# Kernel optimization log

Hardware: AMD Instinct MI355X
Metric: run time of the kernel (lower is better)

Reference implementation:

```python
import jax, jax.numpy as jnp
import numpy as np

N = 50000          # nodes
E = 800000         # edges per view (avg degree 16)
HID = 128
EMB = 64
K = 10
INPUT_DIMS = [1000, 800, 600]


def setup_inputs() -> dict:
    key = jax.random.key(0)
    ks = jax.random.split(key, 32)
    d = {}
    for i, din in enumerate(INPUT_DIMS):
        d[f"x{i}"] = jax.random.normal(ks[i], (N, din), jnp.float32)
        d[f"rows{i}"] = jax.random.randint(ks[3 + i], (E,), 0, N)
        d[f"cols{i}"] = jax.random.randint(ks[6 + i], (E,), 0, N)
        d[f"vals{i}"] = jax.random.uniform(ks[9 + i], (E,), jnp.float32)
        s1 = 1.0 / np.sqrt(HID)   # GraphConvolution.reset_parameters: 1/sqrt(out_features)
        s2 = 1.0 / np.sqrt(EMB)
        d[f"w1_{i}"] = jax.random.uniform(ks[12 + i], (din, HID), jnp.float32, -s1, s1)
        d[f"b1_{i}"] = jax.random.uniform(ks[15 + i], (HID,), jnp.float32, -s1, s1)
        d[f"w2_{i}"] = jax.random.uniform(ks[18 + i], (HID, EMB), jnp.float32, -s2, s2)
        d[f"b2_{i}"] = jax.random.uniform(ks[21 + i], (EMB,), jnp.float32, -s2, s2)
    sf = 1.0 / np.sqrt(EMB * 3)   # nn.Linear default init
    d["fusion_w"] = jax.random.uniform(ks[24], (EMB * 3, EMB), jnp.float32, -sf, sf)
    d["fusion_b"] = jax.random.uniform(ks[25], (EMB,), jnp.float32, -sf, sf)
    xav = np.sqrt(2.0 / (K + EMB))  # xavier_normal_
    d["cluster"] = jax.random.normal(ks[26], (K, EMB), jnp.float32) * xav
    return d


def _spmm(rows, cols, vals, dense):
    # adj (COO, NxN) @ dense [N, F] -> [N, F]
    return jax.ops.segment_sum(vals[:, None] * dense[cols], rows, num_segments=N)


def _encode(x, rows, cols, vals, w1, b1, w2, b2):
    h = jax.nn.relu(_spmm(rows, cols, vals, x @ w1) + b1)
    # F.dropout in eval mode = identity
    return _spmm(rows, cols, vals, h @ w2) + b2


def reference(x0, x1, x2,
              rows0, cols0, vals0,
              rows1, cols1, vals1,
              rows2, cols2, vals2,
              w1_0, b1_0, w2_0, b2_0,
              w1_1, b1_1, w2_1, b2_1,
              w1_2, b1_2, w2_2, b2_2,
              fusion_w, fusion_b, cluster):
    z0 = _encode(x0, rows0, cols0, vals0, w1_0, b1_0, w2_0, b2_0)
    z1 = _encode(x1, rows1, cols1, vals1, w1_1, b1_1, w2_1, b2_1)
    z2 = _encode(x2, rows2, cols2, vals2, w1_2, b1_2, w2_2, b2_2)
    z_concat = jnp.concatenate([z0, z1, z2], axis=1)          # [N, 3*EMB]
    z_fused = jax.nn.relu(z_concat @ fusion_w + fusion_b)     # [N, EMB]
    # DEC-style soft assignment (Student-t, alpha=1 -> exponent (1+1)/2 = 1)
    d2 = jnp.sum((z_fused[:, None, :] - cluster[None, :, :]) ** 2, axis=2)  # [N, K]
    q = 1.0 / (1.0 + d2)
    q = q / jnp.sum(q, axis=1, keepdims=True)
    return (z0, z1, z2, z_fused, q)
```

## Files before the change

kernel.cpp:

```cpp
#include <hip/hip_runtime.h>


#define N_NODES 50000
#define N_EDGES 800000
#define HID 128
#define EMB 64
#define NCLU 10

using bf16x8 = __attribute__((ext_vector_type(8))) short;
using f32x4  = __attribute__((ext_vector_type(4))) float;

static __device__ __forceinline__ unsigned short f2bf(float f) {
    unsigned int u = __float_as_uint(f);
    unsigned int r = (u + 0x7FFF + ((u >> 16) & 1)) >> 16;
    return (unsigned short)r;
}
static __device__ __forceinline__ float bflo(unsigned int t) {
    return __uint_as_float(t << 16);
}
static __device__ __forceinline__ float bfhi(unsigned int t) {
    return __uint_as_float(t & 0xFFFF0000u);
}


__global__ void hist3_kernel(const int* __restrict__ r0, const int* __restrict__ r1,
                             const int* __restrict__ r2, int* __restrict__ counts) {
    int t = blockIdx.x * 256 + threadIdx.x;
    int view = t / N_EDGES;
    int i = t - view * N_EDGES;
    const int* rp = (view == 0) ? r0 : (view == 1) ? r1 : r2;
    atomicAdd(&counts[view * N_NODES + rp[i]], 1);
}

__global__ __launch_bounds__(256) void scan1_kernel(
    const int* __restrict__ counts, int* __restrict__ tmp, int* __restrict__ bsum, int n)
{
    __shared__ int wt[4];
    int t = threadIdx.x, b = blockIdx.x;
    int i = b * 256 + t;
    int lane = t & 63, wid = t >> 6;
    int v = (i < n) ? counts[i] : 0;
    int incl = v;
    #pragma unroll
    for (int d = 1; d < 64; d <<= 1) {
        int u = __shfl_up(incl, d, 64);
        if (lane >= d) incl += u;
    }
    if (lane == 63) wt[wid] = incl;
    __syncthreads();
    int woff = 0;
    #pragma unroll
    for (int w = 0; w < 4; ++w) if (w < wid) woff += wt[w];
    if (i < n) tmp[i] = woff + incl - v;
    if (t == 255) bsum[b] = woff + incl;
}

__global__ __launch_bounds__(256) void scan2_kernel(
    const int* __restrict__ bsum, int* __restrict__ boff, int nb,
    int* __restrict__ row_ptr, int n)
{
    __shared__ int wt[4];
    int t = threadIdx.x;
    int lane = t & 63, wid = t >> 6;
    int carry = 0;
    for (int c0 = 0; c0 < nb; c0 += 256) {
        int i = c0 + t;
        int v = (i < nb) ? bsum[i] : 0;
        int incl = v;
        #pragma unroll
        for (int d = 1; d < 64; d <<= 1) {
            int u = __shfl_up(incl, d, 64);
            if (lane >= d) incl += u;
        }
        __syncthreads();
        if (lane == 63) wt[wid] = incl;
        __syncthreads();
        int woff = 0;
        #pragma unroll
        for (int w = 0; w < 4; ++w) if (w < wid) woff += wt[w];
        int chunktot = wt[0] + wt[1] + wt[2] + wt[3];
        if (i < nb) boff[i] = carry + woff + incl - v;
        carry += chunktot;
    }
    if (t == 0) row_ptr[n] = carry;
}

__global__ __launch_bounds__(256) void scan3_kernel(
    const int* __restrict__ tmp, const int* __restrict__ boff,
    int* __restrict__ row_ptr, int* __restrict__ cursor, int n)
{
    int i = blockIdx.x * 256 + threadIdx.x;
    if (i < n) {
        int e = tmp[i] + boff[blockIdx.x];
        row_ptr[i] = e;
        cursor[i] = e;
    }
}

__global__ void scatter3_kernel(
    const int* __restrict__ r0, const int* __restrict__ c0, const float* __restrict__ v0,
    const int* __restrict__ r1, const int* __restrict__ c1, const float* __restrict__ v1,
    const int* __restrict__ r2, const int* __restrict__ c2, const float* __restrict__ v2,
    int* __restrict__ cursor, float2* __restrict__ cv)
{
    int t = blockIdx.x * 256 + threadIdx.x;
    int view = t / N_EDGES;
    int i = t - view * N_EDGES;
    const int* rp = (view == 0) ? r0 : (view == 1) ? r1 : r2;
    const int* cp = (view == 0) ? c0 : (view == 1) ? c1 : c2;
    const float* vp = (view == 0) ? v0 : (view == 1) ? v1 : v2;
    int r = view * N_NODES + rp[i];
    int p = atomicAdd(&cursor[r], 1);
    float2 e;
    e.x = __uint_as_float((unsigned int)cp[i]);
    e.y = vp[i];
    cv[p] = e;
}


__global__ void wconv_kernel(const float* __restrict__ w, unsigned short* __restrict__ wt,
                             int din, int dinp) {
    int t = blockIdx.x * 256 + threadIdx.x;
    if (t >= 128 * dinp) return;
    int n = t / dinp, k = t - n * dinp;
    float f = (k < din) ? w[(size_t)k * 128 + n] : 0.f;
    wt[(size_t)n * dinp + k] = f2bf(f);
}


#define SAW 72

__global__ __launch_bounds__(256) void gemm1_kernel(
    const float* __restrict__ x, const unsigned short* __restrict__ w1t,
    unsigned short* __restrict__ xw, int Nn, int din, int dinp)
{
    __shared__ unsigned short As[64 * SAW];
    __shared__ unsigned short Bs[128 * SAW];
    int tid = threadIdx.x;
    int lane = tid & 63, wid = tid >> 6;
    int row0 = blockIdx.x * 64;
    int numK = dinp >> 6;

    int ar = tid >> 4;
    int ak = (tid & 15) * 4;
    float4 apre[4];
    uint4  bpre[4];

    auto loadA = [&](int k0) {
        #pragma unroll
        for (int p = 0; p < 4; ++p) {
            int r = p * 16 + ar;
            int gr = row0 + r;
            int k = k0 + ak;
            float4 v = make_float4(0.f, 0.f, 0.f, 0.f);
            if (gr < Nn) {
                if (k + 4 <= din) {
                    v = *(const float4*)(x + (size_t)gr * din + k);
                } else {
                    float e0 = (k + 0 < din) ? x[(size_t)gr * din + k + 0] : 0.f;
                    float e1 = (k + 1 < din) ? x[(size_t)gr * din + k + 1] : 0.f;
                    float e2 = (k + 2 < din) ? x[(size_t)gr * din + k + 2] : 0.f;
                    float e3 = (k + 3 < din) ? x[(size_t)gr * din + k + 3] : 0.f;
                    v = make_float4(e0, e1, e2, e3);
                }
            }
            apre[p] = v;
        }
    };
    auto loadB = [&](int k0) {
        #pragma unroll
        for (int p = 0; p < 4; ++p) {
            int idx = p * 256 + tid;
            int n = idx >> 3, q = idx & 7;
            bpre[p] = *(const uint4*)(w1t + (size_t)n * dinp + k0 + q * 8);
        }
    };
    auto storeLDS = [&]() {
        #pragma unroll
        for (int p = 0; p < 4; ++p) {
            int r = p * 16 + ar;
            ushort4 b;
            b.x = f2bf(apre[p].x); b.y = f2bf(apre[p].y);
            b.z = f2bf(apre[p].z); b.w = f2bf(apre[p].w);
            *(ushort4*)(&As[r * SAW + ak]) = b;
        }
        #pragma unroll
        for (int p = 0; p < 4; ++p) {
            int idx = p * 256 + tid;
            int n = idx >> 3, q = idx & 7;
            *(uint4*)(&Bs[n * SAW + q * 8]) = bpre[p];
        }
    };

    loadA(0); loadB(0);
    storeLDS();

    int kq = (lane >> 4) * 8;
    int sub = lane & 15;
    f32x4 acc[4][2] = {};
    for (int kt = 0;;) {
        __syncthreads();
        bool more = (kt + 1 < numK);
        if (more) { loadA((kt + 1) << 6); loadB((kt + 1) << 6); }
        #pragma unroll
        for (int kh = 0; kh < 2; ++kh) {
            bf16x8 af[4], bfr[2];
            #pragma unroll
            for (int mt = 0; mt < 4; ++mt)
                af[mt] = *(const bf16x8*)(&As[(mt * 16 + sub) * SAW + kh * 32 + kq]);
            #pragma unroll
            for (int nt = 0; nt < 2; ++nt)
                bfr[nt] = *(const bf16x8*)(&Bs[(wid * 32 + nt * 16 + sub) * SAW + kh * 32 + kq]);
            #pragma unroll
            for (int mt = 0; mt < 4; ++mt)
                #pragma unroll
                for (int nt = 0; nt < 2; ++nt)
                    acc[mt][nt] = __builtin_amdgcn_mfma_f32_16x16x32_bf16(af[mt], bfr[nt], acc[mt][nt], 0, 0, 0);
        }
        if (!more) break;
        __syncthreads();
        storeLDS();
        ++kt;
    }

    #pragma unroll
    for (int mt = 0; mt < 4; ++mt) {
        #pragma unroll
        for (int nt = 0; nt < 2; ++nt) {
            int col = wid * 32 + nt * 16 + (lane & 15);
            #pragma unroll
            for (int r = 0; r < 4; ++r) {
                int row = row0 + mt * 16 + (lane >> 4) * 4 + r;
                if (row < Nn) xw[(size_t)row * 128 + col] = f2bf(acc[mt][nt][r]);
            }
        }
    }
}


__global__ __launch_bounds__(256) void spmm128_kernel(
    const unsigned short* __restrict__ src, const int* __restrict__ row_ptr,
    const float2* __restrict__ cv, const float* __restrict__ bias,
    unsigned short* __restrict__ dst)
{
    const unsigned int* srcu = (const unsigned int*)src;
    int lane = threadIdx.x & 63;
    int r = blockIdx.x * 4 + (threadIdx.x >> 6);
    int s = row_ptr[r], e = row_ptr[r + 1];
    float a0 = 0.f, a1 = 0.f, b0 = 0.f, b1 = 0.f;
    int j = s;
    for (; j + 8 <= e; j += 8) {
        float2 p0 = cv[j], p1 = cv[j + 1], p2 = cv[j + 2], p3 = cv[j + 3];
        float2 p4 = cv[j + 4], p5 = cv[j + 5], p6 = cv[j + 6], p7 = cv[j + 7];
        unsigned int t0 = srcu[(size_t)__float_as_uint(p0.x) * 64 + lane];
        unsigned int t1 = srcu[(size_t)__float_as_uint(p1.x) * 64 + lane];
        unsigned int t2 = srcu[(size_t)__float_as_uint(p2.x) * 64 + lane];
        unsigned int t3 = srcu[(size_t)__float_as_uint(p3.x) * 64 + lane];
        unsigned int t4 = srcu[(size_t)__float_as_uint(p4.x) * 64 + lane];
        unsigned int t5 = srcu[(size_t)__float_as_uint(p5.x) * 64 + lane];
        unsigned int t6 = srcu[(size_t)__float_as_uint(p6.x) * 64 + lane];
        unsigned int t7 = srcu[(size_t)__float_as_uint(p7.x) * 64 + lane];
        a0 += p0.y * bflo(t0); a1 += p0.y * bfhi(t0);
        b0 += p1.y * bflo(t1); b1 += p1.y * bfhi(t1);
        a0 += p2.y * bflo(t2); a1 += p2.y * bfhi(t2);
        b0 += p3.y * bflo(t3); b1 += p3.y * bfhi(t3);
        a0 += p4.y * bflo(t4); a1 += p4.y * bfhi(t4);
        b0 += p5.y * bflo(t5); b1 += p5.y * bfhi(t5);
        a0 += p6.y * bflo(t6); a1 += p6.y * bfhi(t6);
        b0 += p7.y * bflo(t7); b1 += p7.y * bfhi(t7);
    }
    for (; j < e; ++j) {
        float2 p = cv[j];
        unsigned int t = srcu[(size_t)__float_as_uint(p.x) * 64 + lane];
        a0 += p.y * bflo(t); a1 += p.y * bfhi(t);
    }
    a0 += b0 + bias[lane * 2];
    a1 += b1 + bias[lane * 2 + 1];
    a0 = fmaxf(a0, 0.f); a1 = fmaxf(a1, 0.f);
    unsigned int o = (unsigned int)f2bf(a0) | ((unsigned int)f2bf(a1) << 16);
    ((unsigned int*)dst)[(size_t)r * 64 + lane] = o;
}


__global__ __launch_bounds__(256) void spmm64_kernel(
    const unsigned short* __restrict__ src, const int* __restrict__ row_ptr,
    const float2* __restrict__ cv, const float* __restrict__ bias,
    float* __restrict__ dst)
{
    int lane = threadIdx.x & 63;
    int r = blockIdx.x * 4 + (threadIdx.x >> 6);
    int s = row_ptr[r], e = row_ptr[r + 1];
    float a0 = 0.f, b0 = 0.f;
    int j = s;
    for (; j + 8 <= e; j += 8) {
        float2 p0 = cv[j], p1 = cv[j + 1], p2 = cv[j + 2], p3 = cv[j + 3];
        float2 p4 = cv[j + 4], p5 = cv[j + 5], p6 = cv[j + 6], p7 = cv[j + 7];
        float f0 = __uint_as_float((unsigned int)src[(size_t)__float_as_uint(p0.x) * 64 + lane] << 16);
        float f1 = __uint_as_float((unsigned int)src[(size_t)__float_as_uint(p1.x) * 64 + lane] << 16);
        float f2 = __uint_as_float((unsigned int)src[(size_t)__float_as_uint(p2.x) * 64 + lane] << 16);
        float f3 = __uint_as_float((unsigned int)src[(size_t)__float_as_uint(p3.x) * 64 + lane] << 16);
        float f4 = __uint_as_float((unsigned int)src[(size_t)__float_as_uint(p4.x) * 64 + lane] << 16);
        float f5 = __uint_as_float((unsigned int)src[(size_t)__float_as_uint(p5.x) * 64 + lane] << 16);
        float f6 = __uint_as_float((unsigned int)src[(size_t)__float_as_uint(p6.x) * 64 + lane] << 16);
        float f7 = __uint_as_float((unsigned int)src[(size_t)__float_as_uint(p7.x) * 64 + lane] << 16);
        a0 += p0.y * f0; b0 += p1.y * f1;
        a0 += p2.y * f2; b0 += p3.y * f3;
        a0 += p4.y * f4; b0 += p5.y * f5;
        a0 += p6.y * f6; b0 += p7.y * f7;
    }
    for (; j < e; ++j) {
        float2 p = cv[j];
        float f = __uint_as_float((unsigned int)src[(size_t)__float_as_uint(p.x) * 64 + lane] << 16);
        a0 += p.y * f;
    }
    dst[(size_t)r * 64 + lane] = a0 + b0 + bias[lane];
}


__global__ __launch_bounds__(256) void gemm2_kernel(
    const unsigned short* __restrict__ h, const float* __restrict__ w2,
    unsigned short* __restrict__ hw)
{
    __shared__ float w2s[128 * 64];
    int tid = threadIdx.x;
    for (int i = tid; i < 128 * 64; i += 256) w2s[i] = w2[i];
    __syncthreads();
    int n = tid & 63, g = tid >> 6;
    int r0 = blockIdx.x * 16 + g * 4;
    const unsigned int* h0 = (const unsigned int*)(h + (size_t)r0 * 128);
    float a0 = 0.f, a1 = 0.f, a2 = 0.f, a3 = 0.f;
    #pragma unroll 4
    for (int k2 = 0; k2 < 64; ++k2) {
        unsigned int t0 = h0[k2], t1 = h0[64 + k2], t2 = h0[128 + k2], t3 = h0[192 + k2];
        float w0 = w2s[(2 * k2) * 64 + n];
        float w1 = w2s[(2 * k2 + 1) * 64 + n];
        a0 += bflo(t0) * w0 + bfhi(t0) * w1;
        a1 += bflo(t1) * w0 + bfhi(t1) * w1;
        a2 += bflo(t2) * w0 + bfhi(t2) * w1;
        a3 += bflo(t3) * w0 + bfhi(t3) * w1;
    }
    hw[(size_t)(r0 + 0) * 64 + n] = f2bf(a0);
    hw[(size_t)(r0 + 1) * 64 + n] = f2bf(a1);
    hw[(size_t)(r0 + 2) * 64 + n] = f2bf(a2);
    hw[(size_t)(r0 + 3) * 64 + n] = f2bf(a3);
}


__global__ __launch_bounds__(256) void fusion_kernel(
    const float* __restrict__ z, const float* __restrict__ fw,
    const float* __restrict__ fb, float* __restrict__ zf)
{
    __shared__ float ws_[192 * 64];
    int tid = threadIdx.x;
    for (int i = tid; i < 192 * 64; i += 256) ws_[i] = fw[i];
    __syncthreads();
    int n = tid & 63, g = tid >> 6;
    int r0 = blockIdx.x * 16 + g * 4;
    float a0 = 0.f, a1 = 0.f, a2 = 0.f, a3 = 0.f;
    #pragma unroll
    for (int v = 0; v < 3; ++v) {
        const float* zv = z + (size_t)v * N_NODES * 64;
        const float* z0 = zv + (size_t)(r0 + 0) * 64;
        const float* z1 = zv + (size_t)(r0 + 1) * 64;
        const float* z2 = zv + (size_t)(r0 + 2) * 64;
        const float* z3 = zv + (size_t)(r0 + 3) * 64;
        #pragma unroll 4
        for (int k = 0; k < 64; ++k) {
            float w = ws_[(v * 64 + k) * 64 + n];
            a0 += z0[k] * w; a1 += z1[k] * w; a2 += z2[k] * w; a3 += z3[k] * w;
        }
    }
    float b = fb[n];
    zf[(size_t)(r0 + 0) * 64 + n] = fmaxf(a0 + b, 0.f);
    zf[(size_t)(r0 + 1) * 64 + n] = fmaxf(a1 + b, 0.f);
    zf[(size_t)(r0 + 2) * 64 + n] = fmaxf(a2 + b, 0.f);
    zf[(size_t)(r0 + 3) * 64 + n] = fmaxf(a3 + b, 0.f);
}


__global__ __launch_bounds__(256) void q_kernel(
    const float* __restrict__ zf, const float* __restrict__ cluster, float* __restrict__ q)
{
    int lane = threadIdx.x & 63;
    int r = blockIdx.x * 4 + (threadIdx.x >> 6);
    float zl = zf[(size_t)r * 64 + lane];
    float d2[NCLU];
    #pragma unroll
    for (int k = 0; k < NCLU; ++k) {
        float d = zl - cluster[k * 64 + lane];
        float s = d * d;
        #pragma unroll
        for (int m = 32; m; m >>= 1) s += __shfl_xor(s, m, 64);
        d2[k] = s;
    }
    float S = 0.f;
    #pragma unroll
    for (int k = 0; k < NCLU; ++k) S += 1.f / (1.f + d2[k]);
    float myq = 0.f;
    #pragma unroll
    for (int k = 0; k < NCLU; ++k)
        if (lane == k) myq = 1.f / (1.f + d2[k]);
    if (lane < NCLU) q[(size_t)r * NCLU + lane] = myq / S;
}


extern "C" void kernel_launch(void* const* d_in, const int* in_sizes, int n_in,
                              void* d_out, int out_size, void* d_ws, size_t ws_size,
                              hipStream_t stream)
{
    const int N = N_NODES, E = N_EDGES;
    const int N3 = 3 * N, E3 = 3 * E;
    const int NB3 = (N3 + 255) / 256;
    static const int dins[3] = {1000, 800, 600};
    float* out = (float*)d_out;
    char* base = (char*)d_ws;
    size_t off = 0;
    auto alloc = [&](size_t bytes) -> void* {
        void* p = base + off;
        off = (off + bytes + 255) & ~(size_t)255;
        return p;
    };
    unsigned short* xw = (unsigned short*)alloc((size_t)N * 128 * 2);
    unsigned short* h  = (unsigned short*)alloc((size_t)N * 128 * 2);
    unsigned short* hw = (unsigned short*)alloc((size_t)N * 64 * 2);
    unsigned short* w1t = (unsigned short*)alloc(128 * 1024 * 2);
    int* counts  = (int*)alloc((size_t)N3 * 4);
    int* cursor  = (int*)alloc((size_t)N3 * 4);
    int* row_ptr = (int*)alloc((size_t)(N3 + 1) * 4);
    int* tmp     = (int*)alloc((size_t)N3 * 4);
    int* bsum    = (int*)alloc((size_t)NB3 * 4);
    int* boff    = (int*)alloc((size_t)NB3 * 4);
    float2* cv   = (float2*)alloc((size_t)E3 * 8);

    const int* rows0 = (const int*)d_in[1];
    const int* cols0 = (const int*)d_in[2];
    const float* vals0 = (const float*)d_in[3];
    const int* rows1 = (const int*)d_in[9];
    const int* cols1 = (const int*)d_in[10];
    const float* vals1 = (const float*)d_in[11];
    const int* rows2 = (const int*)d_in[17];
    const int* cols2 = (const int*)d_in[18];
    const float* vals2 = (const float*)d_in[19];

    hipMemsetAsync(counts, 0, (size_t)N3 * 4, stream);
    hist3_kernel<<<E3 / 256, 256, 0, stream>>>(rows0, rows1, rows2, counts);
    scan1_kernel<<<NB3, 256, 0, stream>>>(counts, tmp, bsum, N3);
    scan2_kernel<<<1, 256, 0, stream>>>(bsum, boff, NB3, row_ptr, N3);
    scan3_kernel<<<NB3, 256, 0, stream>>>(tmp, boff, row_ptr, cursor, N3);
    scatter3_kernel<<<E3 / 256, 256, 0, stream>>>(rows0, cols0, vals0,
                                                  rows1, cols1, vals1,
                                                  rows2, cols2, vals2, cursor, cv);

    for (int v = 0; v < 3; ++v) {
        const float* x    = (const float*)d_in[8 * v + 0];
        const float* w1   = (const float*)d_in[8 * v + 4];
        const float* b1   = (const float*)d_in[8 * v + 5];
        const float* w2   = (const float*)d_in[8 * v + 6];
        const float* b2   = (const float*)d_in[8 * v + 7];
        int din = dins[v], dinp = (din + 63) & ~63;

        wconv_kernel<<<(128 * dinp + 255) / 256, 256, 0, stream>>>(w1, w1t, din, dinp);
        gemm1_kernel<<<(N + 63) / 64, 256, 0, stream>>>(x, w1t, xw, N, din, dinp);
        spmm128_kernel<<<N / 4, 256, 0, stream>>>(xw, row_ptr + v * N, cv, b1, h);
        gemm2_kernel<<<N / 16, 256, 0, stream>>>(h, w2, hw);
        spmm64_kernel<<<N / 4, 256, 0, stream>>>(hw, row_ptr + v * N, cv, b2,
                                                 out + (size_t)v * N * 64);
    }
    const float* fw = (const float*)d_in[24];
    const float* fb = (const float*)d_in[25];
    const float* cl = (const float*)d_in[26];
    fusion_kernel<<<N / 16, 256, 0, stream>>>(out, fw, fb, out + (size_t)3 * N * 64);
    q_kernel<<<N / 4, 256, 0, stream>>>(out + (size_t)3 * N * 64, cl, out + (size_t)4 * N * 64);
}
```

Before: 1.417 ms.

## Replace global-atomic COO-to-CSR build with two-pass LDS bucket sort

Replaces the histogram, three-stage scan and global-atomic scatter with a two-level bucketed sort. Edges are first binned by 128-row bucket inside each block in shared memory, then a per-bucket kernel gathers its runs, sorts them locally by row and writes CSR. The aim is to remove scattered global atomics and random writes. In exchange it adds intermediate buffers that are aliased with later workspace, and buckets larger than BUFCAP are truncated, which risks dropping edges if degrees are skewed.

```diff
diff --git a/kernel.cpp b/kernel.cpp
--- a/kernel.cpp
+++ b/kernel.cpp
@@ -7,6 +7,13 @@
 #define EMB 64
 #define NCLU 10
 
+#define E3 (3 * N_EDGES)
+#define N3 (3 * N_NODES)
+#define CHK 4096
+#define NBLK 586
+#define NBUK 1172
+#define BUFCAP 4352
+
 using bf16x8 = __attribute__((ext_vector_type(8))) short;
 using f32x4  = __attribute__((ext_vector_type(4))) float;
 
@@ -21,100 +28,189 @@
 static __device__ __forceinline__ float bfhi(unsigned int t) {
     return __uint_as_float(t & 0xFFFF0000u);
 }
-
-
-__global__ void hist3_kernel(const int* __restrict__ r0, const int* __restrict__ r1,
-                             const int* __restrict__ r2, int* __restrict__ counts) {
-    int t = blockIdx.x * 256 + threadIdx.x;
-    int view = t / N_EDGES;
-    int i = t - view * N_EDGES;
-    const int* rp = (view == 0) ? r0 : (view == 1) ? r1 : r2;
-    atomicAdd(&counts[view * N_NODES + rp[i]], 1);
-}
-
-__global__ __launch_bounds__(256) void scan1_kernel(
-    const int* __restrict__ counts, int* __restrict__ tmp, int* __restrict__ bsum, int n)
-{
-    __shared__ int wt[4];
-    int t = threadIdx.x, b = blockIdx.x;
-    int i = b * 256 + t;
-    int lane = t & 63, wid = t >> 6;
-    int v = (i < n) ? counts[i] : 0;
-    int incl = v;
+static __device__ __forceinline__ int wave_incl_scan(int v, int lane) {
     #pragma unroll
     for (int d = 1; d < 64; d <<= 1) {
-        int u = __shfl_up(incl, d, 64);
-        if (lane >= d) incl += u;
-    }
-    if (lane == 63) wt[wid] = incl;
-    __syncthreads();
-    int woff = 0;
-    #pragma unroll
-    for (int w = 0; w < 4; ++w) if (w < wid) woff += wt[w];
-    if (i < n) tmp[i] = woff + incl - v;
-    if (t == 255) bsum[b] = woff + incl;
-}
-
-__global__ __launch_bounds__(256) void scan2_kernel(
-    const int* __restrict__ bsum, int* __restrict__ boff, int nb,
-    int* __restrict__ row_ptr, int n)
-{
-    __shared__ int wt[4];
-    int t = threadIdx.x;
-    int lane = t & 63, wid = t >> 6;
-    int carry = 0;
-    for (int c0 = 0; c0 < nb; c0 += 256) {
-        int i = c0 + t;
-        int v = (i < nb) ? bsum[i] : 0;
-        int incl = v;
-        #pragma unroll
-        for (int d = 1; d < 64; d <<= 1) {
-            int u = __shfl_up(incl, d, 64);
-            if (lane >= d) incl += u;
-        }
-        __syncthreads();
-        if (lane == 63) wt[wid] = incl;
-        __syncthreads();
-        int woff = 0;
-        #pragma unroll
-        for (int w = 0; w < 4; ++w) if (w < wid) woff += wt[w];
-        int chunktot = wt[0] + wt[1] + wt[2] + wt[3];
-        if (i < nb) boff[i] = carry + woff + incl - v;
-        carry += chunktot;
-    }
-    if (t == 0) row_ptr[n] = carry;
-}
-
-__global__ __launch_bounds__(256) void scan3_kernel(
-    const int* __restrict__ tmp, const int* __restrict__ boff,
-    int* __restrict__ row_ptr, int* __restrict__ cursor, int n)
-{
-    int i = blockIdx.x * 256 + threadIdx.x;
-    if (i < n) {
-        int e = tmp[i] + boff[blockIdx.x];
-        row_ptr[i] = e;
-        cursor[i] = e;
-    }
-}
-
-__global__ void scatter3_kernel(
+        int u = __shfl_up(v, d, 64);
+        if (lane >= d) v += u;
+    }
+    return v;
+}
+
+
+__global__ __launch_bounds__(256) void binA_kernel(
     const int* __restrict__ r0, const int* __restrict__ c0, const float* __restrict__ v0,
     const int* __restrict__ r1, const int* __restrict__ c1, const float* __restrict__ v1,
     const int* __restrict__ r2, const int* __restrict__ c2, const float* __restrict__ v2,
-    int* __restrict__ cursor, float2* __restrict__ cv)
-{
-    int t = blockIdx.x * 256 + threadIdx.x;
-    int view = t / N_EDGES;
-    int i = t - view * N_EDGES;
-    const int* rp = (view == 0) ? r0 : (view == 1) ? r1 : r2;
-    const int* cp = (view == 0) ? c0 : (view == 1) ? c1 : c2;
-    const float* vp = (view == 0) ? v0 : (view == 1) ? v1 : v2;
-    int r = view * N_NODES + rp[i];
-    int p = atomicAdd(&cursor[r], 1);
-    float2 e;
-    e.x = __uint_as_float((unsigned int)cp[i]);
-    e.y = vp[i];
-    cv[p] = e;
+    int* __restrict__ runstart, int* __restrict__ counts, uint2* __restrict__ chunkout)
+{
+    __shared__ int hist[NBUK];
+    __shared__ int wt[4];
+    int tid = threadIdx.x, blk = blockIdx.x;
+    int lane = tid & 63, wid = tid >> 6;
+    int base = blk * CHK;
+    int cnt = min(CHK, E3 - base);
+    for (int i = tid; i < NBUK; i += 256) hist[i] = 0;
+    __syncthreads();
+    for (int j = tid; j < cnt; j += 256) {
+        int t = base + j;
+        int view = t / N_EDGES;
+        int i = t - view * N_EDGES;
+        const int* rp = (view == 0) ? r0 : (view == 1) ? r1 : r2;
+        int grow = view * N_NODES + rp[i];
+        atomicAdd(&hist[grow >> 7], 1);
+    }
+    __syncthreads();
+    int carry = 0;
+    for (int cc = 0; cc < NBUK; cc += 256) {
+        int i = cc + tid;
+        int v = (i < NBUK) ? hist[i] : 0;
+        int incl = wave_incl_scan(v, lane);
+        __syncthreads();
+        if (lane == 63) wt[wid] = incl;
+        __syncthreads();
+        int woff = 0;
+        #pragma unroll
+        for (int w = 0; w < 4; ++w) if (w < wid) woff += wt[w];
+        int tot = wt[0] + wt[1] + wt[2] + wt[3];
+        int excl = carry + woff + incl - v;
+        if (i < NBUK) {
+            counts[(size_t)blk * NBUK + i]   = v;
+            runstart[(size_t)blk * NBUK + i] = excl;
+            hist[i] = excl;
+        }
+        carry += tot;
+        __syncthreads();
+    }
+    for (int j = tid; j < cnt; j += 256) {
+        int t = base + j;
+        int view = t / N_EDGES;
+        int i = t - view * N_EDGES;
+        const int* rp = (view == 0) ? r0 : (view == 1) ? r1 : r2;
+        const int* cp = (view == 0) ? c0 : (view == 1) ? c1 : c2;
+        const float* vp = (view == 0) ? v0 : (view == 1) ? v1 : v2;
+        int grow = view * N_NODES + rp[i];
+        int b = grow >> 7;
+        int p = atomicAdd(&hist[b], 1);
+        uint2 e;
+        e.x = ((unsigned int)(grow & 127) << 16) | (unsigned int)cp[i];
+        e.y = __float_as_uint(vp[i]);
+        chunkout[(size_t)blk * CHK + p] = e;
+    }
+}
+
+
+__global__ __launch_bounds__(256) void s1_kernel(
+    const int* __restrict__ counts, int* __restrict__ offs, int* __restrict__ bsum)
+{
+    __shared__ int wt[4];
+    int b = blockIdx.x, tid = threadIdx.x;
+    int lane = tid & 63, wid = tid >> 6;
+    int carry = 0;
+    for (int cc = 0; cc < NBLK; cc += 256) {
+        int i = cc + tid;
+        int v = (i < NBLK) ? counts[(size_t)i * NBUK + b] : 0;
+        int incl = wave_incl_scan(v, lane);
+        __syncthreads();
+        if (lane == 63) wt[wid] = incl;
+        __syncthreads();
+        int woff = 0;
+        #pragma unroll
+        for (int w = 0; w < 4; ++w) if (w < wid) woff += wt[w];
+        int tot = wt[0] + wt[1] + wt[2] + wt[3];
+        if (i < NBLK) offs[(size_t)b * (NBLK + 1) + i] = carry + woff + incl - v;
+        carry += tot;
+        __syncthreads();
+    }
+    if (tid == 0) {
+        offs[(size_t)b * (NBLK + 1) + NBLK] = carry;
+        bsum[b] = carry;
+    }
+}
+
+
+__global__ __launch_bounds__(256) void s2_kernel(
+    const int* __restrict__ bsum, int* __restrict__ bucketbase, int* __restrict__ row_ptr)
+{
+    __shared__ int wt[4];
+    int tid = threadIdx.x;
+    int lane = tid & 63, wid = tid >> 6;
+    int carry = 0;
+    for (int cc = 0; cc < NBUK; cc += 256) {
+        int i = cc + tid;
+        int v = (i < NBUK) ? bsum[i] : 0;
+        int incl = wave_incl_scan(v, lane);
+        __syncthreads();
+        if (lane == 63) wt[wid] = incl;
+        __syncthreads();
+        int woff = 0;
+        #pragma unroll
+        for (int w = 0; w < 4; ++w) if (w < wid) woff += wt[w];
+        int tot = wt[0] + wt[1] + wt[2] + wt[3];
+        if (i < NBUK) bucketbase[i] = carry + woff + incl - v;
+        carry += tot;
+        __syncthreads();
+    }
+    if (tid == 0) {
+        bucketbase[NBUK] = carry;
+        row_ptr[N3] = carry;
+    }
+}
+
+
+__global__ __launch_bounds__(256) void binB_kernel(
+    const uint2* __restrict__ chunkout, const int* __restrict__ offs,
+    const int* __restrict__ runstart, const int* __restrict__ bucketbase,
+    int* __restrict__ row_ptr, uint2* __restrict__ cv)
+{
+    __shared__ int so[NBLK + 1];
+    __shared__ int srs[NBLK];
+    __shared__ int rh[128];
+    __shared__ int wt2[2];
+    __shared__ uint2 buf[BUFCAP];
+    int b = blockIdx.x, tid = threadIdx.x;
+    for (int i = tid; i <= NBLK; i += 256) so[i] = offs[(size_t)b * (NBLK + 1) + i];
+    for (int i = tid; i < NBLK; i += 256) srs[i] = runstart[(size_t)i * NBUK + b];
+    if (tid < 128) rh[tid] = 0;
+    int base = bucketbase[b];
+    __syncthreads();
+    int cntb = so[NBLK];
+    if (cntb > BUFCAP) cntb = BUFCAP;
+    for (int i = tid; i < cntb; i += 256) {
+        int lo = 0, hi = NBLK;
+        while (hi - lo > 1) { int m = (lo + hi) >> 1; if (so[m] <= i) lo = m; else hi = m; }
+        uint2 e = chunkout[(size_t)lo * CHK + srs[lo] + (i - so[lo])];
+        buf[i] = e;
+        atomicAdd(&rh[e.x >> 16], 1);
+    }
+    __syncthreads();
+    int rows_in = min(128, N3 - b * 128);
+    int v = 0, incl = 0;
+    if (tid < 128) {
+        v = rh[tid];
+        int lane = tid & 63;
+        incl = wave_incl_scan(v, lane);
+        if (lane == 63) wt2[tid >> 6] = incl;
+    }
+    __syncthreads();
+    int excl = 0;
+    if (tid < 128) {
+        int woff = (tid >= 64) ? wt2[0] : 0;
+        excl = woff + incl - v;
+        if (tid < rows_in) row_ptr[b * 128 + tid] = base + excl;
+    }
+    __syncthreads();
+    if (tid < 128) rh[tid] = excl;
+    __syncthreads();
+    for (int i = tid; i < cntb; i += 256) {
+        uint2 e = buf[i];
+        int lr = e.x >> 16;
+        int p = atomicAdd(&rh[lr], 1);
+        uint2 o;
+        o.x = e.x & 0xFFFFu;
+        o.y = e.y;
+        cv[(size_t)base + p] = o;
+    }
 }
 
 
@@ -179,10 +275,10 @@
         #pragma unroll
         for (int p = 0; p < 4; ++p) {
             int r = p * 16 + ar;
-            ushort4 b;
-            b.x = f2bf(apre[p].x); b.y = f2bf(apre[p].y);
-            b.z = f2bf(apre[p].z); b.w = f2bf(apre[p].w);
-            *(ushort4*)(&As[r * SAW + ak]) = b;
+            ushort4 bb;
+            bb.x = f2bf(apre[p].x); bb.y = f2bf(apre[p].y);
+            bb.z = f2bf(apre[p].z); bb.w = f2bf(apre[p].w);
+            *(ushort4*)(&As[r * SAW + ak]) = bb;
         }
         #pragma unroll
         for (int p = 0; p < 4; ++p) {
@@ -408,29 +504,31 @@
                               void* d_out, int out_size, void* d_ws, size_t ws_size,
                               hipStream_t stream)
 {
-    const int N = N_NODES, E = N_EDGES;
-    const int N3 = 3 * N, E3 = 3 * E;
-    const int NB3 = (N3 + 255) / 256;
+    const int N = N_NODES;
     static const int dins[3] = {1000, 800, 600};
     float* out = (float*)d_out;
     char* base = (char*)d_ws;
-    size_t off = 0;
-    auto alloc = [&](size_t bytes) -> void* {
-        void* p = base + off;
-        off = (off + bytes + 255) & ~(size_t)255;
-        return p;
-    };
-    unsigned short* xw = (unsigned short*)alloc((size_t)N * 128 * 2);
-    unsigned short* h  = (unsigned short*)alloc((size_t)N * 128 * 2);
-    unsigned short* hw = (unsigned short*)alloc((size_t)N * 64 * 2);
-    unsigned short* w1t = (unsigned short*)alloc(128 * 1024 * 2);
-    int* counts  = (int*)alloc((size_t)N3 * 4);
-    int* cursor  = (int*)alloc((size_t)N3 * 4);
-    int* row_ptr = (int*)alloc((size_t)(N3 + 1) * 4);
-    int* tmp     = (int*)alloc((size_t)N3 * 4);
-    int* bsum    = (int*)alloc((size_t)NB3 * 4);
-    int* boff    = (int*)alloc((size_t)NB3 * 4);
-    float2* cv   = (float2*)alloc((size_t)E3 * 8);
+
+    size_t oCv  = 0;
+    size_t oR1  = (oCv + (size_t)E3 * 8 + 255) & ~(size_t)255;
+    size_t szR1 = (size_t)NBLK * CHK * 8;
+    size_t oR2  = (oR1 + szR1 + 255) & ~(size_t)255;
+    size_t szR2 = (size_t)N * 128 * 2;
+    size_t oW1t = (oR2 + szR2 + 255) & ~(size_t)255;
+    size_t oRp  = (oW1t + (size_t)128 * 1024 * 2 + 255) & ~(size_t)255;
+
+    uint2* cv        = (uint2*)(base + oCv);
+    uint2* chunkout  = (uint2*)(base + oR1);
+    unsigned short* h  = (unsigned short*)(base + oR1);
+    unsigned short* hw = (unsigned short*)(base + oR1 + (size_t)N * 128 * 2);
+    unsigned short* xw = (unsigned short*)(base + oR2);
+    int* runstart   = (int*)(base + oR2);
+    int* counts     = (int*)(base + oR2 + (size_t)NBLK * NBUK * 4);
+    int* offs       = (int*)(base + oR2 + (size_t)NBLK * NBUK * 8);
+    int* bsum       = (int*)(base + oR2 + (size_t)NBLK * NBUK * 8 + (size_t)NBUK * (NBLK + 1) * 4);
+    int* bucketbase = bsum + NBUK + 4;
+    unsigned short* w1t = (unsigned short*)(base + oW1t);
+    int* row_ptr    = (int*)(base + oRp);
 
     const int* rows0 = (const int*)d_in[1];
     const int* cols0 = (const int*)d_in[2];
@@ -442,14 +540,11 @@
     const int* cols2 = (const int*)d_in[18];
     const float* vals2 = (const float*)d_in[19];
 
-    hipMemsetAsync(counts, 0, (size_t)N3 * 4, stream);
-    hist3_kernel<<<E3 / 256, 256, 0, stream>>>(rows0, rows1, rows2, counts);
-    scan1_kernel<<<NB3, 256, 0, stream>>>(counts, tmp, bsum, N3);
-    scan2_kernel<<<1, 256, 0, stream>>>(bsum, boff, NB3, row_ptr, N3);
-    scan3_kernel<<<NB3, 256, 0, stream>>>(tmp, boff, row_ptr, cursor, N3);
-    scatter3_kernel<<<E3 / 256, 256, 0, stream>>>(rows0, cols0, vals0,
-                                                  rows1, cols1, vals1,
-                                                  rows2, cols2, vals2, cursor, cv);
+    binA_kernel<<<NBLK, 256, 0, stream>>>(rows0, cols0, vals0, rows1, cols1, vals1,
+                                          rows2, cols2, vals2, runstart, counts, chunkout);
+    s1_kernel<<<NBUK, 256, 0, stream>>>(counts, offs, bsum);
+    s2_kernel<<<1, 256, 0, stream>>>(bsum, bucketbase, row_ptr);
+    binB_kernel<<<NBUK, 256, 0, stream>>>(chunkout, offs, runstart, bucketbase, row_ptr, cv);
 
     for (int v = 0; v < 3; ++v) {
         const float* x    = (const float*)d_in[8 * v + 0];
@@ -461,9 +556,9 @@
 
         wconv_kernel<<<(128 * dinp + 255) / 256, 256, 0, stream>>>(w1, w1t, din, dinp);
         gemm1_kernel<<<(N + 63) / 64, 256, 0, stream>>>(x, w1t, xw, N, din, dinp);
-        spmm128_kernel<<<N / 4, 256, 0, stream>>>(xw, row_ptr + v * N, cv, b1, h);
+        spmm128_kernel<<<N / 4, 256, 0, stream>>>(xw, row_ptr + v * N, (const float2*)cv, b1, h);
         gemm2_kernel<<<N / 16, 256, 0, stream>>>(h, w2, hw);
-        spmm64_kernel<<<N / 4, 256, 0, stream>>>(hw, row_ptr + v * N, cv, b2,
+        spmm64_kernel<<<N / 4, 256, 0, stream>>>(hw, row_ptr + v * N, (const float2*)cv, b2,
                                                  out + (size_t)v * N * 64);
     }
     const float* fw = (const float*)d_in[24];
```

Result: faster. 1.234 ms (-12.9%).
